# Performance work log

Hardware: AMD Instinct MI355X
Metric: run time of the kernel (lower is better)

## Reference

```python
import jax, jax.numpy as jnp
import numpy as np

N = 65536   # number of input points
M = 4096    # subsample_size (centroids)
K = 64      # group_limit (neighborhood size)
RADIUS = 0.2  # group_radius


def _mlp(x, W1, b1, W2, b2, W3, b3):
    # PyG MLP([6, 64, 64, 128], act='relu'); batch_norm with default running
    # stats (mean 0, var 1) is identity, so: Linear-ReLU-Linear-ReLU-Linear.
    h = jax.nn.relu(x @ W1 + b1)
    h = jax.nn.relu(h @ W2 + b2)
    return h @ W3 + b3


def setup_inputs() -> dict:
    key = jax.random.key(0)
    ks = jax.random.split(key, 8)
    vertices = jax.random.normal(ks[0], (N, 3), dtype=jnp.float32)
    centroid_indices = jax.random.randint(ks[1], (M,), 0, N)

    def lin(k, fi, fo):
        return (jax.random.normal(k, (fi, fo), dtype=jnp.float32) / np.sqrt(fi)).astype(jnp.float32)

    return {
        "vertices": vertices,
        "centroid_indices": centroid_indices,
        "W1": lin(ks[2], 6, 64),  "b1": jnp.zeros((64,), jnp.float32),
        "W2": lin(ks[3], 64, 64), "b2": jnp.zeros((64,), jnp.float32),
        "W3": lin(ks[4], 64, 128), "b3": jnp.zeros((128,), jnp.float32),
    }


def reference(vertices, centroid_indices, W1, b1, W2, b2, W3, b3):
    # --- group_around_centroids ---
    sq_norm = jnp.einsum('ij,ij->i', vertices, vertices)          # [N]
    cpos = vertices[centroid_indices]                              # [M,3]
    # faithful distance formula: sqrt(|sn_c - 2 c.v + sn|)
    d = jnp.sqrt(jnp.abs(sq_norm[centroid_indices][:, None]
                         - 2.0 * (cpos @ vertices.T)
                         + sq_norm[None, :]))                      # [M,N]  (~1 GB)
    # K nearest per centroid (equivalent to masking by k-th sorted distance)
    neg_dk, idx = jax.lax.top_k(-d, K)                             # [M,K]
    d_k = -neg_dk                                                  # ascending distances
    limit = jnp.minimum(d_k[:, K - 1], RADIUS)                     # [M]
    mask = d_k <= limit[:, None]                                   # [M,K]

    # --- PointNetConv: msg = MLP(cat[x_j, pos_j - pos_i]), max-aggregate to centroid ---
    pos_j = vertices[idx]                                          # [M,K,3]
    feat = jnp.concatenate([pos_j, pos_j - cpos[:, None, :]], axis=-1)  # [M,K,6]
    h = _mlp(feat, W1, b1, W2, b2, W3, b3)                         # [M,K,128]
    h = jnp.where(mask[:, :, None], h, -jnp.inf)
    return jnp.max(h, axis=1)                                      # [M,128]
```

## Files before the change

kernel.cpp:

```cpp
#include <hip/hip_runtime.h>
#include <hip/hip_bf16.h>

#define GD     50
#define NC     (GD*GD*GD)
#define CHUNK  250
#define CAPK   256
#define RADIUS_F 0.2f
#define R2SAFE 0.0401f

typedef unsigned long long ull;
typedef __attribute__((ext_vector_type(4))) _Float16 f16x4;
typedef __attribute__((ext_vector_type(8))) _Float16 f16x8;
typedef __attribute__((ext_vector_type(4))) float    f32x4;

__device__ __forceinline__ int cellcoord(float v) {
    int c = (int)floorf((v + 5.0f) * 5.0f);
    return min(max(c, 0), GD - 1);
}


__global__ void sa_zero_kernel(int4* __restrict__ dst, int n4) {
    int i = blockIdx.x * blockDim.x + threadIdx.x;
    int stride = gridDim.x * blockDim.x;
    for (; i < n4; i += stride) dst[i] = make_int4(0, 0, 0, 0);
}

__global__ void sa_prep_kernel(const float* __restrict__ vtx,
                               float4* __restrict__ pt4,
                               int* __restrict__ cid,
                               int* __restrict__ cellCnt,
                               int N,
                               const float* __restrict__ W1,
                               const float* __restrict__ W2,
                               const float* __restrict__ W3,
                               _Float16* __restrict__ wf16) {
    int i = blockIdx.x * blockDim.x + threadIdx.x;
    int stride = gridDim.x * blockDim.x;
    for (int p = i; p < N; p += stride) {
        float x = vtx[3 * p], y = vtx[3 * p + 1], z = vtx[3 * p + 2];
        float sn = fmaf(z, z, fmaf(y, y, x * x));
        pt4[p] = make_float4(x, y, z, sn);
        int cc = (cellcoord(z) * GD + cellcoord(y)) * GD + cellcoord(x);
        cid[p] = cc;
        atomicAdd(&cellCnt[cc], 1);
    }
    for (int e = i; e < 1024; e += stride) {
        int nn = e >> 8, lane = (e >> 2) & 63, j = e & 3;
        int col = nn * 16 + (lane & 15), k = (lane >> 4) * 4 + j;
        wf16[e] = (k < 6) ? (_Float16)W1[k * 64 + col] : (_Float16)0.f;
    }
    for (int e = i; e < 2048; e += stride) {
        int nn = e >> 9, lane = (e >> 3) & 63, j = e & 7;
        int col = nn * 16 + (lane & 15), k = (lane >> 4) * 8 + j;
        wf16[1024 + e] = (_Float16)W2[k * 64 + col];
        wf16[3072 + e] = (_Float16)W2[(k + 32) * 64 + col];
    }
    for (int e = i; e < 4096; e += stride) {
        int nn = e >> 9, lane = (e >> 3) & 63, j = e & 7;
        int col = nn * 16 + (lane & 15), k = (lane >> 4) * 8 + j;
        wf16[5120 + e] = (_Float16)W3[k * 128 + col];
        wf16[9216 + e] = (_Float16)W3[(k + 32) * 128 + col];
    }
}

__global__ __launch_bounds__(256) void sa_offsets_kernel(
    const int* __restrict__ cellCnt, int* __restrict__ cellStart,
    int* __restrict__ cellEnd, int* __restrict__ cellCur,
    int* __restrict__ cursor) {
    __shared__ int sc[256];
    __shared__ int base_s;
    int t = threadIdx.x;
    int i = blockIdx.x * CHUNK + t;
    int c = (t < CHUNK) ? cellCnt[i] : 0;
    sc[t] = c;
    __syncthreads();
    for (int d = 1; d < 256; d <<= 1) {
        int o = (t >= d) ? sc[t - d] : 0;
        __syncthreads();
        sc[t] += o;
        __syncthreads();
    }
    if (t == 255) base_s = atomicAdd(cursor, sc[255]);
    __syncthreads();
    int start = base_s + sc[t] - c;
    if (t < CHUNK) {
        cellStart[i] = start;
        cellEnd[i] = start + c;
        cellCur[i] = start;
    }
}

__global__ void sa_scatter_kernel(const float4* __restrict__ pt4,
                                  const int* __restrict__ cid,
                                  int* __restrict__ cellCur,
                                  float4* __restrict__ sorted4,
                                  int* __restrict__ sidx,
                                  const int* __restrict__ cidx,
                                  float4* __restrict__ cpos4,
                                  int N, int M) {
    int p = blockIdx.x * blockDim.x + threadIdx.x;
    if (p < N) {
        int pos = atomicAdd(&cellCur[cid[p]], 1);
        sorted4[pos] = pt4[p];
        sidx[pos] = p;
    }
    if (p < M) cpos4[p] = pt4[cidx[p]];
}

__global__ __launch_bounds__(64) void sa_collect_kernel(
    const float4* __restrict__ cpos4,
    const float4* __restrict__ sorted4, const int* __restrict__ sidx,
    const int* __restrict__ cellStart, const int* __restrict__ cellEnd,
    int* __restrict__ selG, int* __restrict__ nselG) {

    __shared__ __align__(16) ull key[CAPK + 64];
    __shared__ int selb[64];
    __shared__ int chdesc[64];
    __shared__ int scnt_s;

    int lane = threadIdx.x;
    int c = blockIdx.x;
    float4 cc = cpos4[c];

    int cx = cellcoord(cc.x), cy = cellcoord(cc.y), cz = cellcoord(cc.z);
    int x0 = max(cx - 1, 0), x1 = min(cx + 1, GD - 1), lx = x1 - x0 + 1;
    int y0 = max(cy - 1, 0), y1 = min(cy + 1, GD - 1), ly = y1 - y0 + 1;
    int z0 = max(cz - 1, 0), z1 = min(cz + 1, GD - 1), lz = z1 - z0 + 1;
    int nrow = ly * lz;

    int rstart = 0, rlen = 0;
    if (lane < nrow) {
        int iy = lane % ly, iz = lane / ly;
        int gy = y0 + iy, gz = z0 + iz;
        float ylo = (gy == 0) ? -1e30f : gy * 0.2f - 5.0f;
        float yhi = (gy == GD - 1) ? 1e30f : (gy + 1) * 0.2f - 5.0f;
        float zlo = (gz == 0) ? -1e30f : gz * 0.2f - 5.0f;
        float zhi = (gz == GD - 1) ? 1e30f : (gz + 1) * 0.2f - 5.0f;
        float dy = fmaxf(0.f, fmaxf(ylo - cc.y, cc.y - yhi));
        float dz = fmaxf(0.f, fmaxf(zlo - cc.z, cc.z - zhi));
        if (fmaf(dz, dz, dy * dy) <= R2SAFE) {
            int cell0 = (gz * GD + gy) * GD + x0;
            int cellL = cell0 + (lx - 1);
            rstart = cellStart[cell0];
            rlen = cellEnd[cellL] - rstart;
        }
    }
    if (lane == 0) scnt_s = 0;

    int nch = (rlen + 63) >> 6;
    int ip = nch;
#pragma unroll
    for (int d = 1; d < 16; d <<= 1) {
        int o = __shfl_up(ip, d);
        if (lane >= d) ip += o;
    }
    int C = __shfl(ip, nrow - 1);
    int ebase = ip - nch;
    if (lane < nrow) {
        for (int k = 0; k < nch; ++k) {
            int st = rstart + (k << 6);
            int ln = min(64, rlen - (k << 6));
            chdesc[ebase + k] = st | (ln << 20);
        }
    }

#pragma unroll 2
    for (int ch = 0; ch < C; ++ch) {
        int d0 = chdesc[ch];
        int st = d0 & 0xFFFFF, ln = d0 >> 20;
        if (lane < ln) {
            int sp = st + lane;
            float4 p = sorted4[sp];
            int pid = sidx[sp];
            float dot = fmaf(p.z, cc.z, fmaf(p.y, cc.y, p.x * cc.x));
            float tt = fmaf(-2.f, dot, cc.w) + p.w;
            if (tt <= R2SAFE) {
                float dd = sqrtf(fabsf(tt));
                if (dd <= RADIUS_F) {
                    int slot = atomicAdd(&scnt_s, 1);
                    if (slot < CAPK)
                        key[slot] = (((ull)__float_as_uint(dd)) << 32) | (unsigned)pid;
                }
            }
        }
    }

    int n = min(scnt_s, CAPK);
    int nsel = min(n, 64);
    int n64 = (n + 63) & ~63;
    if (lane < n64 - n) key[n + lane] = ~0ull;
    if (n > 64) {
        for (int i = lane; i < n; i += 64) {
            ull ki = key[i];
            int r = 0;
            for (int j = 0; j < n64; j += 8) {
#pragma unroll
                for (int jj = 0; jj < 8; ++jj)
                    r += (key[j + jj] < ki) ? 1 : 0;
            }
            if (r < 64) selb[r] = (int)(unsigned)(ki & 0xffffffffu);
        }
    } else {
        for (int i = lane; i < n; i += 64)
            selb[i] = (int)(unsigned)(key[i] & 0xffffffffu);
    }

    if (lane < nsel) selG[(size_t)c * 64 + lane] = selb[lane];
    if (lane == 0) nselG[c] = nsel;
}

__global__ __launch_bounds__(256) void sa_mlp3_kernel(
    const float4* __restrict__ pt4, const float4* __restrict__ cpos4,
    const int* __restrict__ selG, const int* __restrict__ nselG,
    const _Float16* __restrict__ wf16,
    const float* __restrict__ b1, const float* __restrict__ b2,
    const float* __restrict__ b3, float* __restrict__ out) {

    __shared__ __align__(16) _Float16 Wf[13312];
    __shared__ __align__(16) float    Wb[256];
    __shared__ __align__(16) _Float16 featb[4][1024];
    __shared__ __align__(16) _Float16 hb[4][4096];

    int t = threadIdx.x, w = t >> 6, lane = t & 63;
    int r16 = lane & 15, g = lane >> 4;
    int c = blockIdx.x * 4 + w;

    {
        const uint4* src = (const uint4*)wf16;
        uint4* dst = (uint4*)Wf;
        for (int i = t; i < 13312 / 8; i += 256) dst[i] = src[i];
        if (t < 64) Wb[t] = b1[t];
        else if (t < 128) Wb[t] = b2[t - 64];
        else Wb[t] = b3[t - 128];
    }
    int nsel = nselG[c];
    float4 cc = cpos4[c];
    {
        _Float16 z = (_Float16)0.f;
        f16x8 lo8 = {z, z, z, z, z, z, z, z};
        if (lane < nsel) {
            float4 p = pt4[selG[(size_t)c * 64 + lane]];
            lo8[0] = (_Float16)p.x; lo8[1] = (_Float16)p.y; lo8[2] = (_Float16)p.z;
            lo8[3] = (_Float16)(p.x - cc.x);
            lo8[4] = (_Float16)(p.y - cc.y);
            lo8[5] = (_Float16)(p.z - cc.z);
        }
        f16x8 hi8 = {z, z, z, z, z, z, z, z};
        *(f16x8*)&featb[w][lane * 16 + 0] = lo8;
        *(f16x8*)&featb[w][lane * 16 + 8] = hi8;
    }
    __syncthreads();

    _Float16* h = hb[w];

    {
        f16x4 a1[4];
#pragma unroll
        for (int m = 0; m < 4; ++m)
            a1[m] = *(const f16x4*)&featb[w][(m * 16 + r16) * 16 + g * 4];
#pragma unroll
        for (int nn = 0; nn < 4; ++nn) {
            int col = nn * 16 + r16;
            f16x4 b = *(const f16x4*)&Wf[(nn * 64 + lane) * 4];
            float bb = Wb[col];
#pragma unroll
            for (int m = 0; m < 4; ++m) {
                f32x4 acc = {bb, bb, bb, bb};
                acc = __builtin_amdgcn_mfma_f32_16x16x16f16(a1[m], b, acc, 0, 0, 0);
#pragma unroll
                for (int reg = 0; reg < 4; ++reg) {
                    int row = m * 16 + g * 4 + reg;
                    h[row * 64 + (col ^ ((row & 7) << 3))] =
                        (_Float16)fmaxf(acc[reg], 0.f);
                }
            }
        }
    }

    {
        f16x8 a2[4][2];
#pragma unroll
        for (int m = 0; m < 4; ++m)
#pragma unroll
            for (int kt = 0; kt < 2; ++kt) {
                int row = m * 16 + r16;
                int k0 = kt * 32 + g * 8;
                a2[m][kt] = *(const f16x8*)&h[row * 64 + (k0 ^ ((row & 7) << 3))];
            }
#pragma unroll
        for (int nn = 0; nn < 4; ++nn) {
            int col = nn * 16 + r16;
            f16x8 bA = *(const f16x8*)&Wf[1024 + (nn * 64 + lane) * 8];
            f16x8 bB = *(const f16x8*)&Wf[3072 + (nn * 64 + lane) * 8];
            float bb = Wb[64 + col];
#pragma unroll
            for (int m = 0; m < 4; ++m) {
                f32x4 acc = {bb, bb, bb, bb};
                acc = __builtin_amdgcn_mfma_f32_16x16x32_f16(a2[m][0], bA, acc, 0, 0, 0);
                acc = __builtin_amdgcn_mfma_f32_16x16x32_f16(a2[m][1], bB, acc, 0, 0, 0);
#pragma unroll
                for (int reg = 0; reg < 4; ++reg) {
                    int row = m * 16 + g * 4 + reg;
                    h[row * 64 + (col ^ ((row & 7) << 3))] =
                        (_Float16)fmaxf(acc[reg], 0.f);
                }
            }
        }
    }

    {
        f16x8 a3[4][2];
#pragma unroll
        for (int m = 0; m < 4; ++m)
#pragma unroll
            for (int kt = 0; kt < 2; ++kt) {
                int row = m * 16 + r16;
                int k0 = kt * 32 + g * 8;
                a3[m][kt] = *(const f16x8*)&h[row * 64 + (k0 ^ ((row & 7) << 3))];
            }
        float ninf = __int_as_float(0xff800000);
#pragma unroll
        for (int nn = 0; nn < 8; ++nn) {
            int col = nn * 16 + r16;
            f16x8 bA = *(const f16x8*)&Wf[5120 + (nn * 64 + lane) * 8];
            f16x8 bB = *(const f16x8*)&Wf[9216 + (nn * 64 + lane) * 8];
            float bb = Wb[128 + col];
            float vm = ninf;
#pragma unroll
            for (int m = 0; m < 4; ++m) {
                f32x4 acc = {bb, bb, bb, bb};
                acc = __builtin_amdgcn_mfma_f32_16x16x32_f16(a3[m][0], bA, acc, 0, 0, 0);
                acc = __builtin_amdgcn_mfma_f32_16x16x32_f16(a3[m][1], bB, acc, 0, 0, 0);
#pragma unroll
                for (int reg = 0; reg < 4; ++reg) {
                    int row = m * 16 + g * 4 + reg;
                    if (row < nsel) vm = fmaxf(vm, acc[reg]);
                }
            }
            vm = fmaxf(vm, __shfl_xor(vm, 16));
            vm = fmaxf(vm, __shfl_xor(vm, 32));
            if (lane < 16) out[(size_t)c * 128 + nn * 16 + lane] = vm;
        }
    }
}

extern "C" void kernel_launch(void* const* d_in, const int* in_sizes, int n_in,
                              void* d_out, int out_size, void* d_ws, size_t ws_size,
                              hipStream_t stream) {
    const float* vtx = (const float*)d_in[0];
    const int* cidx  = (const int*)d_in[1];
    const float* W1  = (const float*)d_in[2];
    const float* b1  = (const float*)d_in[3];
    const float* W2  = (const float*)d_in[4];
    const float* b2  = (const float*)d_in[5];
    const float* W3  = (const float*)d_in[6];
    const float* b3  = (const float*)d_in[7];
    float* out = (float*)d_out;

    int N = in_sizes[0] / 3;
    int M = in_sizes[1];

    char* ws = (char*)d_ws;
    size_t off = 0;
    float4* pt4     = (float4*)(ws + off); off += (size_t)N * 16;
    float4* sorted4 = (float4*)(ws + off); off += (size_t)N * 16;
    float4* cpos4   = (float4*)(ws + off); off += (size_t)M * 16;
    int* sidx       = (int*)(ws + off);    off += (size_t)N * 4;
    int* cid        = (int*)(ws + off);    off += (size_t)N * 4;
    int* cellCnt    = (int*)(ws + off);    off += (size_t)NC * 4;
    int* cursor     = (int*)(ws + off);    off += 16;
    int* cellStart  = (int*)(ws + off);    off += (size_t)NC * 4;
    int* cellEnd    = (int*)(ws + off);    off += (size_t)NC * 4;
    int* cellCur    = (int*)(ws + off);    off += (size_t)NC * 4;
    int* selG       = (int*)(ws + off);    off += (size_t)M * 64 * 4;
    int* nselG      = (int*)(ws + off);    off += (size_t)M * 4;
    _Float16* wf16  = (_Float16*)(ws + off);

    sa_zero_kernel<<<256, 256, 0, stream>>>((int4*)cellCnt, (NC * 4 + 16) / 16);
    sa_prep_kernel<<<512, 256, 0, stream>>>(vtx, pt4, cid, cellCnt, N,
                                            W1, W2, W3, wf16);
    sa_offsets_kernel<<<NC / CHUNK, 256, 0, stream>>>(cellCnt, cellStart,
                                                      cellEnd, cellCur, cursor);
    sa_scatter_kernel<<<(N + 255) / 256, 256, 0, stream>>>(pt4, cid, cellCur,
                                                           sorted4, sidx,
                                                           cidx, cpos4, N, M);
    sa_collect_kernel<<<M, 64, 0, stream>>>(cpos4, sorted4, sidx,
                                            cellStart, cellEnd, selG, nselG);
    sa_mlp3_kernel<<<M / 4, 256, 0, stream>>>(pt4, cpos4, selG, nselG, wf16,
                                              b1, b2, b3, out);
}
```

Baseline: 71.81 us.

## Fuse neighbor collection and MLP kernels into one wave-per-centroid kernel

Merges the neighbor collect kernel (one 64-thread block per centroid) into the MLP kernel (four centroids per 256-thread block), so each wave gathers its own centroid's neighbors and runs the MLP directly. The selected indices stay in shared memory instead of going through the selG/nselG global buffers, and one kernel launch is removed. To save LDS, the key buffer shares space with the feature and hidden buffers. The cost is that the MLP phase now runs in the same, more divergent blocks as the collect phase, and per-block LDS is larger, which may reduce occupancy.

```diff
diff --git a/kernel.cpp b/kernel.cpp
--- a/kernel.cpp
+++ b/kernel.cpp
@@ -107,20 +107,40 @@
     if (p < M) cpos4[p] = pt4[cidx[p]];
 }
 
-__global__ __launch_bounds__(64) void sa_collect_kernel(
-    const float4* __restrict__ cpos4,
+__global__ __launch_bounds__(256) void sa_fused3_kernel(
+    const float4* __restrict__ pt4, const float4* __restrict__ cpos4,
     const float4* __restrict__ sorted4, const int* __restrict__ sidx,
     const int* __restrict__ cellStart, const int* __restrict__ cellEnd,
-    int* __restrict__ selG, int* __restrict__ nselG) {
-
-    __shared__ __align__(16) ull key[CAPK + 64];
-    __shared__ int selb[64];
-    __shared__ int chdesc[64];
-    __shared__ int scnt_s;
-
-    int lane = threadIdx.x;
-    int c = blockIdx.x;
+    const _Float16* __restrict__ wf16,
+    const float* __restrict__ b1, const float* __restrict__ b2,
+    const float* __restrict__ b3, float* __restrict__ out) {
+
+    __shared__ __align__(16) _Float16 Wf[13312];
+    __shared__ __align__(16) float    Wb[256];
+    __shared__ __align__(16) char smem[4][8192];
+    __shared__ int selb[4][64];
+    __shared__ int chdesc[4][64];
+    __shared__ int scnt_s[4];
+
+    int t = threadIdx.x, w = t >> 6, lane = t & 63;
+    int r16 = lane & 15, g = lane >> 4;
+    int c = blockIdx.x * 4 + w;
+
+    {
+        const uint4* src = (const uint4*)wf16;
+        uint4* dst = (uint4*)Wf;
+        for (int i = t; i < 13312 / 8; i += 256) dst[i] = src[i];
+        if (t < 64) Wb[t] = b1[t];
+        else if (t < 128) Wb[t] = b2[t - 64];
+        else Wb[t] = b3[t - 128];
+        if (t < 4) scnt_s[t] = 0;
+    }
+    __syncthreads();
+
     float4 cc = cpos4[c];
+    ull* key = (ull*)smem[w];
+    _Float16* featb = (_Float16*)(smem[w] + 4096);
+    _Float16* h = (_Float16*)smem[w];
 
     int cx = cellcoord(cc.x), cy = cellcoord(cc.y), cz = cellcoord(cc.z);
     int x0 = max(cx - 1, 0), x1 = min(cx + 1, GD - 1), lx = x1 - x0 + 1;
@@ -145,7 +165,6 @@
             rlen = cellEnd[cellL] - rstart;
         }
     }
-    if (lane == 0) scnt_s = 0;
 
     int nch = (rlen + 63) >> 6;
     int ip = nch;
@@ -160,13 +179,13 @@
         for (int k = 0; k < nch; ++k) {
             int st = rstart + (k << 6);
             int ln = min(64, rlen - (k << 6));
-            chdesc[ebase + k] = st | (ln << 20);
+            chdesc[w][ebase + k] = st | (ln << 20);
         }
     }
 
 #pragma unroll 2
     for (int ch = 0; ch < C; ++ch) {
-        int d0 = chdesc[ch];
+        int d0 = chdesc[w][ch];
         int st = d0 & 0xFFFFF, ln = d0 >> 20;
         if (lane < ln) {
             int sp = st + lane;
@@ -177,7 +196,7 @@
             if (tt <= R2SAFE) {
                 float dd = sqrtf(fabsf(tt));
                 if (dd <= RADIUS_F) {
-                    int slot = atomicAdd(&scnt_s, 1);
+                    int slot = atomicAdd(&scnt_s[w], 1);
                     if (slot < CAPK)
                         key[slot] = (((ull)__float_as_uint(dd)) << 32) | (unsigned)pid;
                 }
@@ -185,7 +204,7 @@
         }
     }
 
-    int n = min(scnt_s, CAPK);
+    int n = min(scnt_s[w], CAPK);
     int nsel = min(n, 64);
     int n64 = (n + 63) & ~63;
     if (lane < n64 - n) key[n + lane] = ~0ull;
@@ -198,66 +217,33 @@
                 for (int jj = 0; jj < 8; ++jj)
                     r += (key[j + jj] < ki) ? 1 : 0;
             }
-            if (r < 64) selb[r] = (int)(unsigned)(ki & 0xffffffffu);
+            if (r < 64) selb[w][r] = (int)(unsigned)(ki & 0xffffffffu);
         }
     } else {
         for (int i = lane; i < n; i += 64)
-            selb[i] = (int)(unsigned)(key[i] & 0xffffffffu);
-    }
-
-    if (lane < nsel) selG[(size_t)c * 64 + lane] = selb[lane];
-    if (lane == 0) nselG[c] = nsel;
-}
-
-__global__ __launch_bounds__(256) void sa_mlp3_kernel(
-    const float4* __restrict__ pt4, const float4* __restrict__ cpos4,
-    const int* __restrict__ selG, const int* __restrict__ nselG,
-    const _Float16* __restrict__ wf16,
-    const float* __restrict__ b1, const float* __restrict__ b2,
-    const float* __restrict__ b3, float* __restrict__ out) {
-
-    __shared__ __align__(16) _Float16 Wf[13312];
-    __shared__ __align__(16) float    Wb[256];
-    __shared__ __align__(16) _Float16 featb[4][1024];
-    __shared__ __align__(16) _Float16 hb[4][4096];
-
-    int t = threadIdx.x, w = t >> 6, lane = t & 63;
-    int r16 = lane & 15, g = lane >> 4;
-    int c = blockIdx.x * 4 + w;
-
-    {
-        const uint4* src = (const uint4*)wf16;
-        uint4* dst = (uint4*)Wf;
-        for (int i = t; i < 13312 / 8; i += 256) dst[i] = src[i];
-        if (t < 64) Wb[t] = b1[t];
-        else if (t < 128) Wb[t] = b2[t - 64];
-        else Wb[t] = b3[t - 128];
-    }
-    int nsel = nselG[c];
-    float4 cc = cpos4[c];
+            selb[w][i] = (int)(unsigned)(key[i] & 0xffffffffu);
+    }
+
     {
         _Float16 z = (_Float16)0.f;
         f16x8 lo8 = {z, z, z, z, z, z, z, z};
         if (lane < nsel) {
-            float4 p = pt4[selG[(size_t)c * 64 + lane]];
+            float4 p = pt4[selb[w][lane]];
             lo8[0] = (_Float16)p.x; lo8[1] = (_Float16)p.y; lo8[2] = (_Float16)p.z;
             lo8[3] = (_Float16)(p.x - cc.x);
             lo8[4] = (_Float16)(p.y - cc.y);
             lo8[5] = (_Float16)(p.z - cc.z);
         }
         f16x8 hi8 = {z, z, z, z, z, z, z, z};
-        *(f16x8*)&featb[w][lane * 16 + 0] = lo8;
-        *(f16x8*)&featb[w][lane * 16 + 8] = hi8;
-    }
-    __syncthreads();
-
-    _Float16* h = hb[w];
+        *(f16x8*)&featb[lane * 16 + 0] = lo8;
+        *(f16x8*)&featb[lane * 16 + 8] = hi8;
+    }
 
     {
         f16x4 a1[4];
 #pragma unroll
         for (int m = 0; m < 4; ++m)
-            a1[m] = *(const f16x4*)&featb[w][(m * 16 + r16) * 16 + g * 4];
+            a1[m] = *(const f16x4*)&featb[(m * 16 + r16) * 16 + g * 4];
 #pragma unroll
         for (int nn = 0; nn < 4; ++nn) {
             int col = nn * 16 + r16;
@@ -372,8 +358,6 @@
     int* cellStart  = (int*)(ws + off);    off += (size_t)NC * 4;
     int* cellEnd    = (int*)(ws + off);    off += (size_t)NC * 4;
     int* cellCur    = (int*)(ws + off);    off += (size_t)NC * 4;
-    int* selG       = (int*)(ws + off);    off += (size_t)M * 64 * 4;
-    int* nselG      = (int*)(ws + off);    off += (size_t)M * 4;
     _Float16* wf16  = (_Float16*)(ws + off);
 
     sa_zero_kernel<<<256, 256, 0, stream>>>((int4*)cellCnt, (NC * 4 + 16) / 16);
@@ -384,8 +368,7 @@
     sa_scatter_kernel<<<(N + 255) / 256, 256, 0, stream>>>(pt4, cid, cellCur,
                                                            sorted4, sidx,
                                                            cidx, cpos4, N, M);
-    sa_collect_kernel<<<M, 64, 0, stream>>>(cpos4, sorted4, sidx,
-                                            cellStart, cellEnd, selG, nselG);
-    sa_mlp3_kernel<<<M / 4, 256, 0, stream>>>(pt4, cpos4, selG, nselG, wf16,
-                                              b1, b2, b3, out);
-}
+    sa_fused3_kernel<<<M / 4, 256, 0, stream>>>(pt4, cpos4, sorted4, sidx,
+                                                cellStart, cellEnd, wf16,
+                                                b1, b2, b3, out);
+}
```

Result: slower. 79.26 us (+10.4%).

## Split MLP output columns across warps per centroid, keep weights in registers

Applied to the files above, without the earlier changes.

The MLP kernel changes from one centroid per wave (four centroids per block) to one centroid per block, with the four waves each computing a slice of the output columns. Each wave loads only its own weight fragments and biases straight into registers, so the per-block staging of all weights into shared memory goes away. Shared-memory use per block drops sharply, which allows more resident blocks. The cost is four times as many blocks, extra block-wide barriers between layers, and a feature/activation gather that is now done by one wave and shared through LDS.

```diff
diff --git a/kernel.cpp b/kernel.cpp
--- a/kernel.cpp
+++ b/kernel.cpp
@@ -209,73 +209,69 @@
     if (lane == 0) nselG[c] = nsel;
 }
 
-__global__ __launch_bounds__(256) void sa_mlp3_kernel(
+__global__ __launch_bounds__(256) void sa_mlp4_kernel(
     const float4* __restrict__ pt4, const float4* __restrict__ cpos4,
     const int* __restrict__ selG, const int* __restrict__ nselG,
     const _Float16* __restrict__ wf16,
     const float* __restrict__ b1, const float* __restrict__ b2,
     const float* __restrict__ b3, float* __restrict__ out) {
 
-    __shared__ __align__(16) _Float16 Wf[13312];
-    __shared__ __align__(16) float    Wb[256];
-    __shared__ __align__(16) _Float16 featb[4][1024];
-    __shared__ __align__(16) _Float16 hb[4][4096];
+    __shared__ __align__(16) _Float16 featb[1024];
+    __shared__ __align__(16) _Float16 h[4096];
 
     int t = threadIdx.x, w = t >> 6, lane = t & 63;
     int r16 = lane & 15, g = lane >> 4;
-    int c = blockIdx.x * 4 + w;
-
-    {
-        const uint4* src = (const uint4*)wf16;
-        uint4* dst = (uint4*)Wf;
-        for (int i = t; i < 13312 / 8; i += 256) dst[i] = src[i];
-        if (t < 64) Wb[t] = b1[t];
-        else if (t < 128) Wb[t] = b2[t - 64];
-        else Wb[t] = b3[t - 128];
-    }
+    int c = blockIdx.x;
     int nsel = nselG[c];
     float4 cc = cpos4[c];
-    {
+
+    f16x4 F1  = ((const f16x4*)wf16)[w * 64 + lane];
+    f16x8 FA2 = ((const f16x8*)(wf16 + 1024))[w * 64 + lane];
+    f16x8 FB2 = ((const f16x8*)(wf16 + 3072))[w * 64 + lane];
+    f16x8 FA3a = ((const f16x8*)(wf16 + 5120))[(2 * w + 0) * 64 + lane];
+    f16x8 FA3b = ((const f16x8*)(wf16 + 5120))[(2 * w + 1) * 64 + lane];
+    f16x8 FB3a = ((const f16x8*)(wf16 + 9216))[(2 * w + 0) * 64 + lane];
+    f16x8 FB3b = ((const f16x8*)(wf16 + 9216))[(2 * w + 1) * 64 + lane];
+    float B1 = b1[w * 16 + r16];
+    float B2 = b2[w * 16 + r16];
+    float B3a = b3[(2 * w + 0) * 16 + r16];
+    float B3b = b3[(2 * w + 1) * 16 + r16];
+
+    if (t < 64) {
         _Float16 z = (_Float16)0.f;
         f16x8 lo8 = {z, z, z, z, z, z, z, z};
-        if (lane < nsel) {
-            float4 p = pt4[selG[(size_t)c * 64 + lane]];
+        if (t < nsel) {
+            float4 p = pt4[selG[(size_t)c * 64 + t]];
             lo8[0] = (_Float16)p.x; lo8[1] = (_Float16)p.y; lo8[2] = (_Float16)p.z;
             lo8[3] = (_Float16)(p.x - cc.x);
             lo8[4] = (_Float16)(p.y - cc.y);
             lo8[5] = (_Float16)(p.z - cc.z);
         }
         f16x8 hi8 = {z, z, z, z, z, z, z, z};
-        *(f16x8*)&featb[w][lane * 16 + 0] = lo8;
-        *(f16x8*)&featb[w][lane * 16 + 8] = hi8;
-    }
-    __syncthreads();
-
-    _Float16* h = hb[w];
+        *(f16x8*)&featb[t * 16 + 0] = lo8;
+        *(f16x8*)&featb[t * 16 + 8] = hi8;
+    }
+    __syncthreads();
 
     {
         f16x4 a1[4];
 #pragma unroll
         for (int m = 0; m < 4; ++m)
-            a1[m] = *(const f16x4*)&featb[w][(m * 16 + r16) * 16 + g * 4];
-#pragma unroll
-        for (int nn = 0; nn < 4; ++nn) {
-            int col = nn * 16 + r16;
-            f16x4 b = *(const f16x4*)&Wf[(nn * 64 + lane) * 4];
-            float bb = Wb[col];
-#pragma unroll
-            for (int m = 0; m < 4; ++m) {
-                f32x4 acc = {bb, bb, bb, bb};
-                acc = __builtin_amdgcn_mfma_f32_16x16x16f16(a1[m], b, acc, 0, 0, 0);
-#pragma unroll
-                for (int reg = 0; reg < 4; ++reg) {
-                    int row = m * 16 + g * 4 + reg;
-                    h[row * 64 + (col ^ ((row & 7) << 3))] =
-                        (_Float16)fmaxf(acc[reg], 0.f);
-                }
-            }
-        }
-    }
+            a1[m] = *(const f16x4*)&featb[(m * 16 + r16) * 16 + g * 4];
+        int col = w * 16 + r16;
+#pragma unroll
+        for (int m = 0; m < 4; ++m) {
+            f32x4 acc = {B1, B1, B1, B1};
+            acc = __builtin_amdgcn_mfma_f32_16x16x16f16(a1[m], F1, acc, 0, 0, 0);
+#pragma unroll
+            for (int reg = 0; reg < 4; ++reg) {
+                int row = m * 16 + g * 4 + reg;
+                h[row * 64 + (col ^ ((row & 7) << 3))] =
+                    (_Float16)fmaxf(acc[reg], 0.f);
+            }
+        }
+    }
+    __syncthreads();
 
     {
         f16x8 a2[4][2];
@@ -287,26 +283,22 @@
                 int k0 = kt * 32 + g * 8;
                 a2[m][kt] = *(const f16x8*)&h[row * 64 + (k0 ^ ((row & 7) << 3))];
             }
-#pragma unroll
-        for (int nn = 0; nn < 4; ++nn) {
-            int col = nn * 16 + r16;
-            f16x8 bA = *(const f16x8*)&Wf[1024 + (nn * 64 + lane) * 8];
-            f16x8 bB = *(const f16x8*)&Wf[3072 + (nn * 64 + lane) * 8];
-            float bb = Wb[64 + col];
-#pragma unroll
-            for (int m = 0; m < 4; ++m) {
-                f32x4 acc = {bb, bb, bb, bb};
-                acc = __builtin_amdgcn_mfma_f32_16x16x32_f16(a2[m][0], bA, acc, 0, 0, 0);
-                acc = __builtin_amdgcn_mfma_f32_16x16x32_f16(a2[m][1], bB, acc, 0, 0, 0);
-#pragma unroll
-                for (int reg = 0; reg < 4; ++reg) {
-                    int row = m * 16 + g * 4 + reg;
-                    h[row * 64 + (col ^ ((row & 7) << 3))] =
-                        (_Float16)fmaxf(acc[reg], 0.f);
-                }
-            }
-        }
-    }
+        __syncthreads();
+        int col = w * 16 + r16;
+#pragma unroll
+        for (int m = 0; m < 4; ++m) {
+            f32x4 acc = {B2, B2, B2, B2};
+            acc = __builtin_amdgcn_mfma_f32_16x16x32_f16(a2[m][0], FA2, acc, 0, 0, 0);
+            acc = __builtin_amdgcn_mfma_f32_16x16x32_f16(a2[m][1], FB2, acc, 0, 0, 0);
+#pragma unroll
+            for (int reg = 0; reg < 4; ++reg) {
+                int row = m * 16 + g * 4 + reg;
+                h[row * 64 + (col ^ ((row & 7) << 3))] =
+                    (_Float16)fmaxf(acc[reg], 0.f);
+            }
+        }
+    }
+    __syncthreads();
 
     {
         f16x8 a3[4][2];
@@ -320,17 +312,16 @@
             }
         float ninf = __int_as_float(0xff800000);
 #pragma unroll
-        for (int nn = 0; nn < 8; ++nn) {
-            int col = nn * 16 + r16;
-            f16x8 bA = *(const f16x8*)&Wf[5120 + (nn * 64 + lane) * 8];
-            f16x8 bB = *(const f16x8*)&Wf[9216 + (nn * 64 + lane) * 8];
-            float bb = Wb[128 + col];
+        for (int q = 0; q < 2; ++q) {
+            float bb = q ? B3b : B3a;
+            f16x8 fa = q ? FA3b : FA3a;
+            f16x8 fb = q ? FB3b : FB3a;
             float vm = ninf;
 #pragma unroll
             for (int m = 0; m < 4; ++m) {
                 f32x4 acc = {bb, bb, bb, bb};
-                acc = __builtin_amdgcn_mfma_f32_16x16x32_f16(a3[m][0], bA, acc, 0, 0, 0);
-                acc = __builtin_amdgcn_mfma_f32_16x16x32_f16(a3[m][1], bB, acc, 0, 0, 0);
+                acc = __builtin_amdgcn_mfma_f32_16x16x32_f16(a3[m][0], fa, acc, 0, 0, 0);
+                acc = __builtin_amdgcn_mfma_f32_16x16x32_f16(a3[m][1], fb, acc, 0, 0, 0);
 #pragma unroll
                 for (int reg = 0; reg < 4; ++reg) {
                     int row = m * 16 + g * 4 + reg;
@@ -339,7 +330,8 @@
             }
             vm = fmaxf(vm, __shfl_xor(vm, 16));
             vm = fmaxf(vm, __shfl_xor(vm, 32));
-            if (lane < 16) out[(size_t)c * 128 + nn * 16 + lane] = vm;
+            if (lane < 16)
+                out[(size_t)c * 128 + (2 * w + q) * 16 + lane] = vm;
         }
     }
 }
@@ -386,6 +378,6 @@
                                                            cidx, cpos4, N, M);
     sa_collect_kernel<<<M, 64, 0, stream>>>(cpos4, sorted4, sidx,
                                             cellStart, cellEnd, selG, nselG);
-    sa_mlp3_kernel<<<M / 4, 256, 0, stream>>>(pt4, cpos4, selG, nselG, wf16,
-                                              b1, b2, b3, out);
-}
+    sa_mlp4_kernel<<<M, 256, 0, stream>>>(pt4, cpos4, selG, nselG, wf16,
+                                          b1, b2, b3, out);
+}
```

Result: faster. 68.42 us (-4.7%).
